# Optimization experiments

Hardware: AMD Instinct MI355X
Metric: run time of the kernel (lower is better)

The kernel has to match this reference:

```python
import jax, jax.numpy as jnp
import numpy as np

LAYERS, BLOCKS = 10, 3
NL = LAYERS * BLOCKS
DC, RC, SC, CLASSES, K = 128, 128, 256, 256, 2
SR = 4096  # number of output samples sliced from the end
N, L, EN = 4, 8192, 16


def _conv1x1(x, w):
    # x: [N, Cin, L], w: [Cout, Cin] -> [N, Cout, L]
    return jnp.einsum('ncl,oc->nol', x, w)


def _condition(x, enc):
    # x: [N, C, L], enc: [N, C, En], L % En == 0; tiled periodic add (faithful to the view trick)
    n, c, l = x.shape
    en = enc.shape[2]
    return (x.reshape(n, c, l // en, en) + enc[:, :, None, :]).reshape(n, c, l)


def _dilated_causal_conv(x, w, d):
    # kernel_size=2 causal dilated conv. x: [N, Cin, L], w: [Cout, Cin, 2]
    xs = jnp.pad(x, ((0, 0), (0, 0), (d, 0)))[:, :, :x.shape[2]]  # x delayed by d
    return jnp.einsum('ncl,oc->nol', xs, w[:, :, 0]) + jnp.einsum('ncl,oc->nol', x, w[:, :, 1])


def setup_inputs() -> dict:
    key = jax.random.key(0)
    ks = jax.random.split(key, 12)
    s = 0.05
    return {
        'x': jax.random.normal(ks[0], (N, CLASSES, L), jnp.float32),
        'en': jax.random.normal(ks[1], (N, CLASSES, EN), jnp.float32),
        'start1_w': jax.random.normal(ks[2], (RC, CLASSES), jnp.float32) * s,
        'start2_w': jax.random.normal(ks[3], (SC, RC), jnp.float32) * s,
        'cond_w': jax.random.normal(ks[4], (NL, 2 * DC, CLASSES), jnp.float32) * s,
        'dil_w': jax.random.normal(ks[5], (NL, 2 * DC, RC, K), jnp.float32) * s,
        'res_w': jax.random.normal(ks[6], (NL, RC, DC), jnp.float32) * s,
        'skip_w': jax.random.normal(ks[7], (NL, SC, DC), jnp.float32) * s,
        'end1_w': jax.random.normal(ks[8], (CLASSES, SC), jnp.float32) * s,
        'end1_b': jnp.zeros((CLASSES,), jnp.float32),
        'end2_w': jax.random.normal(ks[9], (CLASSES, CLASSES), jnp.float32) * s,
        'end2_b': jnp.zeros((CLASSES,), jnp.float32),
    }


def reference(x, en, start1_w, start2_w, cond_w, dil_w, res_w, skip_w,
              end1_w, end1_b, end2_w, end2_b):
    l = _conv1x1(x, start1_w)          # [N, RC, L]
    s = _conv1x1(l, start2_w)          # [N, SC, L]
    for i in range(NL):
        dil = 2 ** (i % LAYERS)
        d = _dilated_causal_conv(l, dil_w[i], dil)      # [N, 2*DC, L]
        d = _condition(d, _conv1x1(en, cond_w[i]))
        g = jax.nn.sigmoid(d[:, :DC]) * jnp.tanh(d[:, DC:])  # gated, [N, DC, L]
        l = l + _conv1x1(g, res_w[i])
        s = s + _conv1x1(g, skip_w[i])
    s = jax.nn.relu(s)
    s = _conv1x1(s, end1_w) + end1_b[None, :, None]
    s = _condition(s, _conv1x1(en, end2_w) + end2_b[None, :, None])
    s = jax.nn.relu(s)
    return s[:, :, -SR:]
```

## Files before the change

### kernel.cpp

```cpp
#include <hip/hip_runtime.h>

typedef __bf16 bf16_t;
typedef __bf16 bf16x8 __attribute__((ext_vector_type(8)));
typedef __bf16 bf16x4 __attribute__((ext_vector_type(4)));
typedef float  f32x4  __attribute__((ext_vector_type(4)));
typedef int    i32x4  __attribute__((ext_vector_type(4)));

#define PL 136
#define PX 264

__device__ __forceinline__ f32x4 mfma16(bf16x8 a, bf16x8 b, f32x4 c) {
    return __builtin_amdgcn_mfma_f32_16x16x32_bf16(a, b, c, 0, 0, 0);
}

__device__ __forceinline__ void conv_elem(const float* __restrict__ src,
                                          bf16_t* __restrict__ dst,
                                          int idx, int M, int K) {
    int MK = M * K;
    int lay = idx / MK;
    int r = idx - lay * MK;
    int j = r & 7, lane = (r >> 3) & 63, rest = r >> 9;
    int KB = K >> 5;
    int kb = rest % KB, mt = rest / KB;
    int m = mt * 16 + (lane & 15);
    int k = kb * 32 + ((lane >> 4) << 3) + j;
    dst[idx] = (bf16_t)src[(size_t)lay * MK + m * K + k];
}

__global__ void k_prep(const float* __restrict__ rw, const float* __restrict__ kw,
                       const float* __restrict__ s1w, const float* __restrict__ s2w,
                       const float* __restrict__ e1w, const float* __restrict__ dwt,
                       const float* __restrict__ cond_w, const float* __restrict__ end2_w,
                       const float* __restrict__ end2_b, const float* __restrict__ en,
                       bf16_t* __restrict__ Ares, bf16_t* __restrict__ Askp,
                       bf16_t* __restrict__ A1, bf16_t* __restrict__ A2,
                       bf16_t* __restrict__ Ae, bf16_t* __restrict__ Adil,
                       float* __restrict__ cond_all, float* __restrict__ cond2) {
    __shared__ f32x4 en_s[1024];
    if (blockIdx.x >= 13952) {
        int bi = blockIdx.x - 13952;
        int i = bi >> 2, n = bi & 3, o = threadIdx.x;
        const f32x4* ep = (const f32x4*)(en + (size_t)n * 4096);
        for (int idx = threadIdx.x; idx < 1024; idx += 256) en_s[idx] = ep[idx];
        __syncthreads();
        const float* W = (i < 30) ? cond_w + ((size_t)i * 256 + o) * 256
                                  : end2_w + (size_t)o * 256;
        f32x4 a0 = {0.f,0.f,0.f,0.f}, a1 = a0, a2 = a0, a3 = a0;
        for (int c = 0; c < 256; c += 4) {
            f32x4 wv = *(const f32x4*)(W + c);
            #pragma unroll
            for (int cc = 0; cc < 4; ++cc) {
                float wf = wv[cc];
                a0 += wf * en_s[(c + cc) * 4 + 0];
                a1 += wf * en_s[(c + cc) * 4 + 1];
                a2 += wf * en_s[(c + cc) * 4 + 2];
                a3 += wf * en_s[(c + cc) * 4 + 3];
            }
        }
        float bias = (i < 30) ? 0.f : end2_b[o];
        float* dst = (i < 30) ? cond_all + (((size_t)i * 4 + n) * 256 + o) * 16
                              : cond2 + ((size_t)n * 256 + o) * 16;
        f32x4* d4 = (f32x4*)dst;
        d4[0] = a0 + bias; d4[1] = a1 + bias; d4[2] = a2 + bias; d4[3] = a3 + bias;
        return;
    }
    int idx = blockIdx.x * 256 + threadIdx.x;
    if (idx < 491520) { conv_elem(rw, Ares, idx, 128, 128); return; }
    idx -= 491520;
    if (idx < 983040) { conv_elem(kw, Askp, idx, 256, 128); return; }
    idx -= 983040;
    if (idx < 32768) { conv_elem(s1w, A1, idx, 128, 256); return; }
    idx -= 32768;
    if (idx < 32768) { conv_elem(s2w, A2, idx, 256, 128); return; }
    idx -= 32768;
    if (idx < 65536) { conv_elem(e1w, Ae, idx, 256, 256); return; }
    idx -= 65536;
    {
        int lay = idx >> 16, r = idx & 65535;
        int j = r & 7, lane = (r >> 3) & 63, rest = r >> 9;
        int kb = rest & 7, mt = rest >> 3;
        int m = mt * 16 + (lane & 15);
        int k = kb * 32 + ((lane >> 4) << 3) + j;
        float v = (k < 128) ? dwt[(((size_t)lay * 256 + m) * 128 + k) * 2]
                            : dwt[(((size_t)lay * 256 + m) * 128 + (k - 128)) * 2 + 1];
        Adil[(size_t)lay * 65536 + r] = (bf16_t)v;
    }
}

__global__ __launch_bounds__(512, 4) void k_start(
    const float* __restrict__ x, bf16_t* __restrict__ la, float* __restrict__ sbuf,
    const bf16_t* __restrict__ A1, const bf16_t* __restrict__ A2, int t_base)
{
    __shared__ __align__(16) bf16_t xt[64 * PX];
    __shared__ __align__(16) bf16_t l0[64 * PL];
    int tid = threadIdx.x;
    int n = blockIdx.y, t0 = t_base + blockIdx.x * 64;
    int lane = tid & 63, w = tid >> 6, i16 = lane & 15, q = lane >> 4;
    f32x4 z = {0.f,0.f,0.f,0.f};
    {
        int t = tid & 63;
        for (int c = tid >> 6; c < 256; c += 8)
            xt[t * PX + c] = (bf16_t)x[((size_t)n * 256 + c) * 8192 + t0 + t];
    }
    __syncthreads();
    f32x4 acc[4] = {z,z,z,z};
    #pragma unroll
    for (int kb = 0; kb < 8; ++kb) {
        int koff = kb * 32 + q * 8;
        bf16x8 bf[4];
        #pragma unroll
        for (int nt = 0; nt < 4; ++nt)
            bf[nt] = *(const bf16x8*)(xt + (nt * 16 + i16) * PX + koff);
        bf16x8 af = *(const bf16x8*)(A1 + (((size_t)w * 8 + kb) * 64 + lane) * 8);
        #pragma unroll
        for (int nt = 0; nt < 4; ++nt) acc[nt] = mfma16(af, bf[nt], acc[nt]);
    }
    #pragma unroll
    for (int nt = 0; nt < 4; ++nt)
        #pragma unroll
        for (int j = 0; j < 4; ++j)
            l0[(nt * 16 + i16) * PL + w * 16 + q * 4 + j] = (bf16_t)acc[nt][j];
    __syncthreads();
    {
        int r = tid >> 4, col = (tid & 15) * 8;
        #pragma unroll
        for (int p = 0; p < 2; ++p) {
            int rr = r + p * 32;
            *(i32x4*)(la + ((size_t)n * 8192 + t0 + rr) * 128 + col) =
                *(const i32x4*)(l0 + rr * PL + col);
        }
    }
    if (t0 >= 4096) {
        f32x4 a2[2][4] = {{z,z,z,z},{z,z,z,z}};
        #pragma unroll
        for (int kb = 0; kb < 4; ++kb) {
            int koff = kb * 32 + q * 8;
            bf16x8 bf[4];
            #pragma unroll
            for (int nt = 0; nt < 4; ++nt)
                bf[nt] = *(const bf16x8*)(l0 + (nt * 16 + i16) * PL + koff);
            #pragma unroll
            for (int mt2 = 0; mt2 < 2; ++mt2) {
                bf16x8 af = *(const bf16x8*)(A2 + ((((size_t)2 * w + mt2) * 4 + kb) * 64 + lane) * 8);
                #pragma unroll
                for (int nt = 0; nt < 4; ++nt) a2[mt2][nt] = mfma16(af, bf[nt], a2[mt2][nt]);
            }
        }
        float* sp = sbuf + (size_t)n * 256 * 4096 + (t0 - 4096);
        #pragma unroll
        for (int mt2 = 0; mt2 < 2; ++mt2)
            #pragma unroll
            for (int nt = 0; nt < 4; ++nt)
                #pragma unroll
                for (int j = 0; j < 4; ++j) {
                    int o = (2 * w + mt2) * 16 + q * 4 + j;
                    sp[(size_t)o * 4096 + nt * 16 + i16] = a2[mt2][nt][j];
                }
    }
}

template<int USEG>
__global__ __launch_bounds__(512, 8) void k_layer(
    const bf16_t* __restrict__ l_in, bf16_t* __restrict__ l_out,
    float* __restrict__ sbuf, bf16_t* __restrict__ Gl,
    const bf16_t* __restrict__ Ad, const bf16_t* __restrict__ Ar,
    const bf16_t* __restrict__ Ak, const float* __restrict__ condL,
    int dil, int t_base, int do_res)
{
    __shared__ __align__(16) bf16_t smA[64 * PL];
    __shared__ __align__(16) bf16_t sm2[32 * PL];
    int tid = threadIdx.x;
    int n = blockIdx.y, t0 = t_base + blockIdx.x * 32;
    int lane = tid & 63, w = tid >> 6, i16 = lane & 15, q = lane >> 4;
    f32x4 z = {0.f,0.f,0.f,0.f};
    const float* cond = condL + (size_t)n * 4096;
    int r = tid >> 4, col = (tid & 15) * 8;
    size_t base = (size_t)n * 8192;
    const bf16_t* curp;
    const bf16_t* delp;
    if (dil < 32) {
        int cnt = (32 + dil) * 16;
        for (int idx = tid; idx < cnt; idx += 512) {
            int rr = idx >> 4, c2 = (idx & 15) * 8;
            *(i32x4*)(smA + rr * PL + c2) =
                *(const i32x4*)(l_in + (base + t0 - dil + rr) * 128 + c2);
        }
        delp = smA; curp = smA + dil * PL;
    } else {
        *(i32x4*)(smA + r * PL + col) =
            *(const i32x4*)(l_in + (base + t0 + r) * 128 + col);
        int gp = t0 - dil + r;
        i32x4 v = {0, 0, 0, 0};
        if (gp >= 0) v = *(const i32x4*)(l_in + (base + gp) * 128 + col);
        *(i32x4*)(smA + (32 + r) * PL + col) = v;
        curp = smA; delp = smA + 32 * PL;
    }
    __syncthreads();

    f32x4 accs[2] = {z,z}, acct[2] = {z,z};
    const bf16x8* AdF = (const bf16x8*)Ad;
    #pragma unroll
    for (int kb = 0; kb < 8; ++kb) {
        const bf16_t* bsrc = (kb < 4) ? delp : curp;
        int koff = (kb & 3) * 32 + q * 8;
        bf16x8 bf[2];
        #pragma unroll
        for (int nt = 0; nt < 2; ++nt)
            bf[nt] = *(const bf16x8*)(bsrc + (nt * 16 + i16) * PL + koff);
        bf16x8 a_s = AdF[((size_t)w * 8 + kb) * 64 + lane];
        bf16x8 a_t = AdF[((size_t)(w + 8) * 8 + kb) * 64 + lane];
        #pragma unroll
        for (int nt = 0; nt < 2; ++nt) {
            accs[nt] = mfma16(a_s, bf[nt], accs[nt]);
            acct[nt] = mfma16(a_t, bf[nt], acct[nt]);
        }
    }
    int c_base = w * 16 + q * 4;
    {
        float cv_s[4], cv_t[4];
        #pragma unroll
        for (int j = 0; j < 4; ++j) {
            cv_s[j] = cond[(c_base + j) * 16 + i16];
            cv_t[j] = cond[(c_base + j + 128) * 16 + i16];
        }
        #pragma unroll
        for (int nt = 0; nt < 2; ++nt) {
            bf16x4 g4;
            #pragma unroll
            for (int j = 0; j < 4; ++j) {
                float vlo = accs[nt][j] + cv_s[j];
                float vhi = acct[nt][j] + cv_t[j];
                float sg = 1.0f / (1.0f + __expf(-vlo));
                float th = 1.0f - 2.0f / (1.0f + __expf(2.0f * vhi));
                g4[j] = (bf16_t)(sg * th);
            }
            *(bf16x4*)(sm2 + (nt * 16 + i16) * PL + c_base) = g4;
        }
    }
    __syncthreads();

    if (USEG) {
        if (t0 >= 4096) {
            int tt = ((tid & 256) >> 4) + (tid & 15);
            int cc = ((tid >> 6) & 3) * 32 + ((tid >> 4) & 3) * 8;
            bf16x8 gv = *(const bf16x8*)(sm2 + tt * PL + cc);
            *(bf16x8*)(Gl + ((size_t)n * 4096 + (t0 - 4096)) * 128 + tid * 8) = gv;
        }
    }

    f32x4 acc2[2] = {z,z};
    const bf16x8* ArF = (const bf16x8*)Ar;
    if (do_res || !USEG) {
        int do_skip = (!USEG) && (t0 >= 4096);
        f32x4 acc3[2][2] = {{z,z},{z,z}};
        const bf16x8* AkF = (const bf16x8*)Ak;
        #pragma unroll
        for (int kb = 0; kb < 4; ++kb) {
            int koff = kb * 32 + q * 8;
            bf16x8 bf[2];
            #pragma unroll
            for (int nt = 0; nt < 2; ++nt)
                bf[nt] = *(const bf16x8*)(sm2 + (nt * 16 + i16) * PL + koff);
            if (do_res) {
                bf16x8 ar = ArF[((size_t)w * 4 + kb) * 64 + lane];
                #pragma unroll
                for (int nt = 0; nt < 2; ++nt) acc2[nt] = mfma16(ar, bf[nt], acc2[nt]);
            }
            if (do_skip) {
                #pragma unroll
                for (int mt2 = 0; mt2 < 2; ++mt2) {
                    bf16x8 ak = AkF[((size_t)(2 * w + mt2) * 4 + kb) * 64 + lane];
                    #pragma unroll
                    for (int nt = 0; nt < 2; ++nt)
                        acc3[mt2][nt] = mfma16(ak, bf[nt], acc3[mt2][nt]);
                }
            }
        }
        if (do_skip) {
            float* sp = sbuf + (size_t)n * 256 * 4096 + (t0 - 4096);
            #pragma unroll
            for (int mt2 = 0; mt2 < 2; ++mt2)
                #pragma unroll
                for (int nt = 0; nt < 2; ++nt)
                    #pragma unroll
                    for (int j = 0; j < 4; ++j) {
                        int o = (2 * w + mt2) * 16 + q * 4 + j;
                        sp[(size_t)o * 4096 + nt * 16 + i16] += acc3[mt2][nt][j];
                    }
        }
    }

    if (do_res) {
        #pragma unroll
        for (int nt = 0; nt < 2; ++nt) {
            int trow = (nt * 16 + i16) * PL;
            bf16x4 lv = *(const bf16x4*)(curp + trow + c_base);
            bf16x4 o4;
            #pragma unroll
            for (int j = 0; j < 4; ++j)
                o4[j] = (bf16_t)((float)lv[j] + acc2[nt][j]);
            *(bf16x4*)(l_out + (base + t0 + nt * 16 + i16) * 128 + c_base) = o4;
        }
    }
}

__global__ __launch_bounds__(512, 4) void k_skip(
    const bf16_t* __restrict__ G, float* __restrict__ sbuf,
    const bf16_t* __restrict__ Askp)
{
    __shared__ __align__(16) bf16_t gbuf[2][8192];
    int tid = threadIdx.x;
    int n = blockIdx.y, t0 = blockIdx.x * 64;
    int lane = tid & 63, w = tid >> 6, i16 = lane & 15, q = lane >> 4;
    f32x4 z = {0.f,0.f,0.f,0.f};
    f32x4 acc[2][4] = {{z,z,z,z},{z,z,z,z}};
    const size_t GLS = (size_t)4 * 4096 * 128;
    const bf16_t* gb = G + ((size_t)n * 4096 + t0) * 128 + tid * 8;
    i32x4 v0[4], v1[4];
    #pragma unroll
    for (int d = 0; d < 4; ++d) {
        v0[d] = *(const i32x4*)(gb + (size_t)d * GLS);
        v1[d] = *(const i32x4*)(gb + (size_t)d * GLS + 4096);
    }
    *(i32x4*)(gbuf[0] + tid * 8) = v0[0];
    *(i32x4*)(gbuf[0] + 4096 + tid * 8) = v1[0];
    v0[0] = *(const i32x4*)(gb + (size_t)4 * GLS);
    v1[0] = *(const i32x4*)(gb + (size_t)4 * GLS + 4096);
    __syncthreads();
    #pragma unroll 1
    for (int i = 0; i < 30; ++i) {
        const bf16x8* AkF = (const bf16x8*)(Askp + (size_t)i * 32768);
        const bf16_t* gB = gbuf[i & 1];
        #pragma unroll
        for (int kb = 0; kb < 4; ++kb) {
            bf16x8 ak0 = AkF[((size_t)(2 * w) * 4 + kb) * 64 + lane];
            bf16x8 ak1 = AkF[((size_t)(2 * w + 1) * 4 + kb) * 64 + lane];
            #pragma unroll
            for (int nt = 0; nt < 4; ++nt) {
                bf16x8 bf = *(const bf16x8*)(gB + (nt >> 1) * 4096 +
                                             (((nt & 1) * 4 + kb) * 64 + lane) * 8);
                acc[0][nt] = mfma16(ak0, bf, acc[0][nt]);
                acc[1][nt] = mfma16(ak1, bf, acc[1][nt]);
            }
        }
        if (i + 1 < 30) {
            int s = (i + 1) & 3;
            bf16_t* db = gbuf[(i + 1) & 1];
            *(i32x4*)(db + tid * 8) = v0[s];
            *(i32x4*)(db + 4096 + tid * 8) = v1[s];
            if (i + 5 < 30) {
                v0[s] = *(const i32x4*)(gb + (size_t)(i + 5) * GLS);
                v1[s] = *(const i32x4*)(gb + (size_t)(i + 5) * GLS + 4096);
            }
            asm volatile("s_waitcnt lgkmcnt(0)" ::: "memory");
            __builtin_amdgcn_sched_barrier(0);
            __builtin_amdgcn_s_barrier();
            __builtin_amdgcn_sched_barrier(0);
        }
    }
    float* sp = sbuf + (size_t)n * 256 * 4096 + t0;
    #pragma unroll
    for (int mt2 = 0; mt2 < 2; ++mt2)
        #pragma unroll
        for (int nt = 0; nt < 4; ++nt)
            #pragma unroll
            for (int j = 0; j < 4; ++j) {
                int o = (2 * w + mt2) * 16 + q * 4 + j;
                sp[(size_t)o * 4096 + nt * 16 + i16] += acc[mt2][nt][j];
            }
}

__global__ __launch_bounds__(512) void k_end(
    const float* __restrict__ sbuf, float* __restrict__ out,
    const bf16_t* __restrict__ Ae, const float* __restrict__ cond2,
    const float* __restrict__ b1)
{
    __shared__ __align__(16) bf16_t st[64 * PX];
    __shared__ float c2[4096];
    __shared__ float b1s[256];
    int tid = threadIdx.x;
    int n = blockIdx.y, t0 = blockIdx.x * 64;
    int lane = tid & 63, w = tid >> 6, i16 = lane & 15, q = lane >> 4;
    f32x4 z = {0.f,0.f,0.f,0.f};
    {
        int t = tid & 63;
        for (int c = tid >> 6; c < 256; c += 8) {
            float v = sbuf[((size_t)n * 256 + c) * 4096 + t0 + t];
            st[t * PX + c] = (bf16_t)fmaxf(v, 0.f);
        }
        const f32x4* cc = (const f32x4*)(cond2 + (size_t)n * 4096);
        for (int idx = tid; idx < 1024; idx += 512) ((f32x4*)c2)[idx] = cc[idx];
        if (tid < 64) ((f32x4*)b1s)[tid] = ((const f32x4*)b1)[tid];
    }
    __syncthreads();
    f32x4 acc[2][4] = {{z,z,z,z},{z,z,z,z}};
    #pragma unroll
    for (int kb = 0; kb < 8; ++kb) {
        int koff = kb * 32 + q * 8;
        bf16x8 bf[4];
        #pragma unroll
        for (int nt = 0; nt < 4; ++nt)
            bf[nt] = *(const bf16x8*)(st + (nt * 16 + i16) * PX + koff);
        #pragma unroll
        for (int mt2 = 0; mt2 < 2; ++mt2) {
            bf16x8 af = *(const bf16x8*)(Ae + ((((size_t)2 * w + mt2) * 8 + kb) * 64 + lane) * 8);
            #pragma unroll
            for (int nt = 0; nt < 4; ++nt) acc[mt2][nt] = mfma16(af, bf[nt], acc[mt2][nt]);
        }
    }
    #pragma unroll
    for (int mt2 = 0; mt2 < 2; ++mt2)
        #pragma unroll
        for (int j = 0; j < 4; ++j) {
            int o = (2 * w + mt2) * 16 + q * 4 + j;
            float bb = b1s[o] + c2[o * 16 + i16];
            #pragma unroll
            for (int nt = 0; nt < 4; ++nt) {
                float v = acc[mt2][nt][j] + bb;
                out[((size_t)n * 256 + o) * 4096 + t0 + nt * 16 + i16] = fmaxf(v, 0.f);
            }
        }
}

extern "C" void kernel_launch(void* const* d_in, const int* in_sizes, int n_in,
                              void* d_out, int out_size, void* d_ws, size_t ws_size,
                              hipStream_t stream) {
    const float* x   = (const float*)d_in[0];
    const float* en  = (const float*)d_in[1];
    const float* s1w = (const float*)d_in[2];
    const float* s2w = (const float*)d_in[3];
    const float* cw  = (const float*)d_in[4];
    const float* dw  = (const float*)d_in[5];
    const float* rw  = (const float*)d_in[6];
    const float* kw  = (const float*)d_in[7];
    const float* e1w = (const float*)d_in[8];
    const float* e1b = (const float*)d_in[9];
    const float* e2w = (const float*)d_in[10];
    const float* e2b = (const float*)d_in[11];
    float* out = (float*)d_out;

    char* p = (char*)d_ws;
    auto take = [&](size_t bytes) {
        char* r = p;
        p += (bytes + 255) & ~(size_t)255;
        return r;
    };
    bf16_t* A1   = (bf16_t*)take((size_t)128 * 256 * 2);
    bf16_t* A2   = (bf16_t*)take((size_t)256 * 128 * 2);
    bf16_t* Ae   = (bf16_t*)take((size_t)256 * 256 * 2);
    bf16_t* Adil = (bf16_t*)take((size_t)30 * 65536 * 2);
    bf16_t* Ares = (bf16_t*)take((size_t)30 * 16384 * 2);
    bf16_t* Askp = (bf16_t*)take((size_t)30 * 32768 * 2);
    float*  condA= (float*)take((size_t)30 * 16384 * 4);
    float*  cond2= (float*)take((size_t)16384 * 4);
    bf16_t* la   = (bf16_t*)take((size_t)4 * 8192 * 128 * 2);
    bf16_t* lb   = (bf16_t*)take((size_t)4 * 8192 * 128 * 2);
    float*  sbuf = (float*)take((size_t)4 * 256 * 4096 * 4);
    bf16_t* G    = (bf16_t*)take((size_t)30 * 4 * 4096 * 128 * 2);
    bool useG = ((size_t)(p - (char*)d_ws) <= ws_size);

    k_prep<<<14076, 256, 0, stream>>>(rw, kw, s1w, s2w, e1w, dw,
                                      cw, e2w, e2b, en,
                                      Ares, Askp, A1, A2, Ae, Adil, condA, cond2);

    int a[30];
    a[29] = 4096;
    for (int i = 28; i >= 0; --i) {
        int nx = a[i + 1] - (1 << ((i + 1) % 10));
        a[i] = nx < 4096 ? (nx & ~63) : 4096;
    }

    k_start<<<dim3(127, 4), 512, 0, stream>>>(x, la, sbuf, A1, A2, 64);

    bf16_t* src = la;
    bf16_t* dst = lb;
    for (int i = 0; i < 30; ++i) {
        dim3 grid((8192 - a[i]) / 32, 4);
        if (useG)
            k_layer<1><<<grid, 512, 0, stream>>>(src, dst, sbuf,
                G + (size_t)i * 4 * 4096 * 128,
                Adil + (size_t)i * 65536, Ares + (size_t)i * 16384,
                Askp + (size_t)i * 32768, condA + (size_t)i * 16384,
                1 << (i % 10), a[i], i < 29 ? 1 : 0);
        else
            k_layer<0><<<grid, 512, 0, stream>>>(src, dst, sbuf, (bf16_t*)nullptr,
                Adil + (size_t)i * 65536, Ares + (size_t)i * 16384,
                Askp + (size_t)i * 32768, condA + (size_t)i * 16384,
                1 << (i % 10), a[i], i < 29 ? 1 : 0);
        bf16_t* t = src; src = dst; dst = t;
    }
    if (useG)
        k_skip<<<dim3(64, 4), 512, 0, stream>>>(G, sbuf, Askp);
    k_end<<<dim3(64, 4), 512, 0, stream>>>(sbuf, out, Ae, cond2, e1b);
}
```

Before: 647.3 us.

## Prefetch weights into registers in layer and skip kernels, lower occupancy bounds

```diff
diff --git a/kernel.cpp b/kernel.cpp
--- a/kernel.cpp
+++ b/kernel.cpp
@@ -160,7 +160,7 @@
 }
 
 template<int USEG>
-__global__ __launch_bounds__(512, 8) void k_layer(
+__global__ __launch_bounds__(512, 4) void k_layer(
     const bf16_t* __restrict__ l_in, bf16_t* __restrict__ l_out,
     float* __restrict__ sbuf, bf16_t* __restrict__ Gl,
     const bf16_t* __restrict__ Ad, const bf16_t* __restrict__ Ar,
@@ -175,7 +175,23 @@
     f32x4 z = {0.f,0.f,0.f,0.f};
     const float* cond = condL + (size_t)n * 4096;
     int r = tid >> 4, col = (tid & 15) * 8;
+    int c_base = w * 16 + q * 4;
     size_t base = (size_t)n * 8192;
+
+    float cv_s[4], cv_t[4];
+    #pragma unroll
+    for (int j = 0; j < 4; ++j) {
+        cv_s[j] = cond[(c_base + j) * 16 + i16];
+        cv_t[j] = cond[(c_base + j + 128) * 16 + i16];
+    }
+    const bf16x8* AdF = (const bf16x8*)Ad;
+    bf16x8 a_s[8], a_t[8];
+    #pragma unroll
+    for (int kb = 0; kb < 8; ++kb) {
+        a_s[kb] = AdF[((size_t)w * 8 + kb) * 64 + lane];
+        a_t[kb] = AdF[((size_t)(w + 8) * 8 + kb) * 64 + lane];
+    }
+
     const bf16_t* curp;
     const bf16_t* delp;
     if (dil < 32) {
@@ -198,7 +214,6 @@
     __syncthreads();
 
     f32x4 accs[2] = {z,z}, acct[2] = {z,z};
-    const bf16x8* AdF = (const bf16x8*)Ad;
     #pragma unroll
     for (int kb = 0; kb < 8; ++kb) {
         const bf16_t* bsrc = (kb < 4) ? delp : curp;
@@ -207,22 +222,22 @@
         #pragma unroll
         for (int nt = 0; nt < 2; ++nt)
             bf[nt] = *(const bf16x8*)(bsrc + (nt * 16 + i16) * PL + koff);
-        bf16x8 a_s = AdF[((size_t)w * 8 + kb) * 64 + lane];
-        bf16x8 a_t = AdF[((size_t)(w + 8) * 8 + kb) * 64 + lane];
         #pragma unroll
         for (int nt = 0; nt < 2; ++nt) {
-            accs[nt] = mfma16(a_s, bf[nt], accs[nt]);
-            acct[nt] = mfma16(a_t, bf[nt], acct[nt]);
-        }
-    }
-    int c_base = w * 16 + q * 4;
-    {
-        float cv_s[4], cv_t[4];
-        #pragma unroll
-        for (int j = 0; j < 4; ++j) {
-            cv_s[j] = cond[(c_base + j) * 16 + i16];
-            cv_t[j] = cond[(c_base + j + 128) * 16 + i16];
-        }
+            accs[nt] = mfma16(a_s[kb], bf[nt], accs[nt]);
+            acct[nt] = mfma16(a_t[kb], bf[nt], acct[nt]);
+        }
+    }
+
+    const bf16x8* ArF = (const bf16x8*)Ar;
+    bf16x8 ar[4];
+    if (do_res) {
+        #pragma unroll
+        for (int kb = 0; kb < 4; ++kb)
+            ar[kb] = ArF[((size_t)w * 4 + kb) * 64 + lane];
+    }
+
+    {
         #pragma unroll
         for (int nt = 0; nt < 2; ++nt) {
             bf16x4 g4;
@@ -249,7 +264,6 @@
     }
 
     f32x4 acc2[2] = {z,z};
-    const bf16x8* ArF = (const bf16x8*)Ar;
     if (do_res || !USEG) {
         int do_skip = (!USEG) && (t0 >= 4096);
         f32x4 acc3[2][2] = {{z,z},{z,z}};
@@ -262,9 +276,8 @@
             for (int nt = 0; nt < 2; ++nt)
                 bf[nt] = *(const bf16x8*)(sm2 + (nt * 16 + i16) * PL + koff);
             if (do_res) {
-                bf16x8 ar = ArF[((size_t)w * 4 + kb) * 64 + lane];
                 #pragma unroll
-                for (int nt = 0; nt < 2; ++nt) acc2[nt] = mfma16(ar, bf[nt], acc2[nt]);
+                for (int nt = 0; nt < 2; ++nt) acc2[nt] = mfma16(ar[kb], bf[nt], acc2[nt]);
             }
             if (do_skip) {
                 #pragma unroll
@@ -304,7 +317,47 @@
     }
 }
 
-__global__ __launch_bounds__(512, 4) void k_skip(
+#define SKIP_HALF(I, AKU, AKP, GW0, GW1)                                        \
+    {                                                                           \
+        const int i_ = (I);                                                     \
+        if (i_ + 1 < 30) {                                                      \
+            bf16_t* db = gbuf[(i_ + 1) & 1];                                    \
+            *(i32x4*)(db + tid * 8) = GW0;                                      \
+            *(i32x4*)(db + 4096 + tid * 8) = GW1;                               \
+        }                                                                       \
+        if (i_ + 3 < 30) {                                                      \
+            const bf16_t* srcp = gb + (size_t)(i_ + 3) * GLS;                   \
+            GW0 = *(const i32x4*)(srcp);                                        \
+            GW1 = *(const i32x4*)(srcp + 4096);                                 \
+        }                                                                       \
+        if (i_ + 1 < 30) {                                                      \
+            const bf16x8* An = (const bf16x8*)(Askp + (size_t)(i_ + 1) * 32768);\
+            _Pragma("unroll")                                                   \
+            for (int kb = 0; kb < 4; ++kb) {                                    \
+                AKP[2 * kb]     = An[fi0 + kb * 64];                            \
+                AKP[2 * kb + 1] = An[fi1 + kb * 64];                            \
+            }                                                                   \
+        }                                                                       \
+        const bf16_t* gp_ = gbuf[i_ & 1];                                       \
+        _Pragma("unroll")                                                       \
+        for (int kb = 0; kb < 4; ++kb) {                                        \
+            _Pragma("unroll")                                                   \
+            for (int nt = 0; nt < 4; ++nt) {                                    \
+                bf16x8 bfv = *(const bf16x8*)(gp_ + (nt >> 1) * 4096 +          \
+                              (((nt & 1) * 4 + kb) * 64 + lane) * 8);           \
+                acc[0][nt] = mfma16(AKU[2 * kb], bfv, acc[0][nt]);              \
+                acc[1][nt] = mfma16(AKU[2 * kb + 1], bfv, acc[1][nt]);          \
+            }                                                                   \
+        }                                                                       \
+        if (i_ + 1 < 30) {                                                      \
+            asm volatile("s_waitcnt lgkmcnt(0)" ::: "memory");                  \
+            __builtin_amdgcn_sched_barrier(0);                                  \
+            __builtin_amdgcn_s_barrier();                                       \
+            __builtin_amdgcn_sched_barrier(0);                                  \
+        }                                                                       \
+    }
+
+__global__ __launch_bounds__(512, 2) void k_skip(
     const bf16_t* __restrict__ G, float* __restrict__ sbuf,
     const bf16_t* __restrict__ Askp)
 {
@@ -316,47 +369,33 @@
     f32x4 acc[2][4] = {{z,z,z,z},{z,z,z,z}};
     const size_t GLS = (size_t)4 * 4096 * 128;
     const bf16_t* gb = G + ((size_t)n * 4096 + t0) * 128 + tid * 8;
-    i32x4 v0[4], v1[4];
-    #pragma unroll
-    for (int d = 0; d < 4; ++d) {
-        v0[d] = *(const i32x4*)(gb + (size_t)d * GLS);
-        v1[d] = *(const i32x4*)(gb + (size_t)d * GLS + 4096);
-    }
-    *(i32x4*)(gbuf[0] + tid * 8) = v0[0];
-    *(i32x4*)(gbuf[0] + 4096 + tid * 8) = v1[0];
-    v0[0] = *(const i32x4*)(gb + (size_t)4 * GLS);
-    v1[0] = *(const i32x4*)(gb + (size_t)4 * GLS + 4096);
+    int fi0 = (2 * w) * 256 + lane;
+    int fi1 = fi0 + 256;
+    bf16x8 akA[8], akB[8];
+    {
+        const bf16x8* A0 = (const bf16x8*)Askp;
+        #pragma unroll
+        for (int kb = 0; kb < 4; ++kb) {
+            akA[2 * kb]     = A0[fi0 + kb * 64];
+            akA[2 * kb + 1] = A0[fi1 + kb * 64];
+        }
+    }
+    i32x4 gA0, gA1, gB0, gB1;
+    {
+        i32x4 t0v = *(const i32x4*)(gb);
+        i32x4 t1v = *(const i32x4*)(gb + 4096);
+        *(i32x4*)(gbuf[0] + tid * 8) = t0v;
+        *(i32x4*)(gbuf[0] + 4096 + tid * 8) = t1v;
+    }
+    gA0 = *(const i32x4*)(gb + 1 * GLS);
+    gA1 = *(const i32x4*)(gb + 1 * GLS + 4096);
+    gB0 = *(const i32x4*)(gb + 2 * GLS);
+    gB1 = *(const i32x4*)(gb + 2 * GLS + 4096);
     __syncthreads();
     #pragma unroll 1
-    for (int i = 0; i < 30; ++i) {
-        const bf16x8* AkF = (const bf16x8*)(Askp + (size_t)i * 32768);
-        const bf16_t* gB = gbuf[i & 1];
-        #pragma unroll
-        for (int kb = 0; kb < 4; ++kb) {
-            bf16x8 ak0 = AkF[((size_t)(2 * w) * 4 + kb) * 64 + lane];
-            bf16x8 ak1 = AkF[((size_t)(2 * w + 1) * 4 + kb) * 64 + lane];
-            #pragma unroll
-            for (int nt = 0; nt < 4; ++nt) {
-                bf16x8 bf = *(const bf16x8*)(gB + (nt >> 1) * 4096 +
-                                             (((nt & 1) * 4 + kb) * 64 + lane) * 8);
-                acc[0][nt] = mfma16(ak0, bf, acc[0][nt]);
-                acc[1][nt] = mfma16(ak1, bf, acc[1][nt]);
-            }
-        }
-        if (i + 1 < 30) {
-            int s = (i + 1) & 3;
-            bf16_t* db = gbuf[(i + 1) & 1];
-            *(i32x4*)(db + tid * 8) = v0[s];
-            *(i32x4*)(db + 4096 + tid * 8) = v1[s];
-            if (i + 5 < 30) {
-                v0[s] = *(const i32x4*)(gb + (size_t)(i + 5) * GLS);
-                v1[s] = *(const i32x4*)(gb + (size_t)(i + 5) * GLS + 4096);
-            }
-            asm volatile("s_waitcnt lgkmcnt(0)" ::: "memory");
-            __builtin_amdgcn_sched_barrier(0);
-            __builtin_amdgcn_s_barrier();
-            __builtin_amdgcn_sched_barrier(0);
-        }
+    for (int ii = 0; ii < 30; ii += 2) {
+        SKIP_HALF(ii,     akA, akB, gA0, gA1)
+        SKIP_HALF(ii + 1, akB, akA, gB0, gB1)
     }
     float* sp = sbuf + (size_t)n * 256 * 4096 + t0;
     #pragma unroll
```

New measurement: 638.9 us. No clear change (-1.3%).
